# Optimization experiments

Measured on AMD Instinct MI355X. Metric: run time of the kernel, lower is better.

## Reference

```python
import jax, jax.numpy as jnp
import numpy as np

ITERS = 3; S = 8; I = 64; E = 64; C = 64; DIN = 128; SLOT = 128; H = 256
B = 64; N = 4096; EPS = 1e-8

def _ln(x, g, b):
    m = jnp.mean(x, -1, keepdims=True)
    v = jnp.var(x, -1, keepdims=True)
    return (x - m) * jax.lax.rsqrt(v + 1e-5) * g + b

def _gru(x, h, Wih, Whh, bih, bhh):
    # torch nn.GRUCell math; W stored as [in, 3*hidden]
    gi = x @ Wih + bih
    gh = h @ Whh + bhh
    ir, iz, inn = jnp.split(gi, 3, -1)
    hr, hz, hn = jnp.split(gh, 3, -1)
    r = jax.nn.sigmoid(ir + hr)
    z = jax.nn.sigmoid(iz + hz)
    n = jnp.tanh(inn + r * hn)
    return (1.0 - z) * n + z * h

def setup_inputs() -> dict:
    k = jax.random.split(jax.random.key(0), 32)
    d = {}
    d['slots_bck'] = jax.random.normal(k[0], (B, 1, SLOT), jnp.float32)
    d['inputs'] = jax.random.normal(k[1], (B, N, DIN), jnp.float32)
    d['protos'] = jax.random.normal(k[2], (C, I), jnp.float32)
    d['ext_noise'] = jax.random.normal(k[3], (B, S, E), jnp.float32)
    d['int_noise'] = jax.random.normal(k[4], (B, S, C), jnp.float32)
    u = jax.random.uniform(k[5], (ITERS, B, S, C), jnp.float32, 1e-6, 1.0 - 1e-6)
    d['gumbel'] = -jnp.log(-jnp.log(u))
    d['tau'] = 1
    w = lambda i, shape, s=0.05: jax.random.normal(k[i], shape, jnp.float32) * s
    d['ext_mu'] = w(6, (1, 1, E)); d['ext_log_sigma'] = w(7, (1, 1, E))
    d['int_mu'] = w(8, (1, 1, C)); d['int_log_sigma'] = w(9, (1, 1, C))
    d['ln_in_g'] = jnp.ones((DIN,)); d['ln_in_b'] = jnp.zeros((DIN,))
    d['ln_p_g'] = jnp.ones((I,)); d['ln_p_b'] = jnp.zeros((I,))
    d['ln_mi_g'] = jnp.ones((I,)); d['ln_mi_b'] = jnp.zeros((I,))
    d['ln_me_g'] = jnp.ones((E,)); d['ln_me_b'] = jnp.zeros((E,))
    d['Wq'] = w(10, (SLOT, SLOT)); d['Wk'] = w(11, (DIN, SLOT))
    d['Wv'] = w(12, (DIN, SLOT)); d['Wp'] = w(13, (I, I))
    d['gi_Wih'] = w(14, (I, 3 * I)); d['gi_Whh'] = w(15, (I, 3 * I))
    d['gi_bih'] = jnp.zeros((3 * I,)); d['gi_bhh'] = jnp.zeros((3 * I,))
    d['ge_Wih'] = w(16, (E, 3 * E)); d['ge_Whh'] = w(17, (E, 3 * E))
    d['ge_bih'] = jnp.zeros((3 * E,)); d['ge_bhh'] = jnp.zeros((3 * E,))
    d['mi_W1'] = w(18, (I, H)); d['mi_b1'] = jnp.zeros((H,))
    d['mi_W2'] = w(19, (H, I)); d['mi_b2'] = jnp.zeros((I,))
    d['me_W1'] = w(20, (E, H)); d['me_b1'] = jnp.zeros((H,))
    d['me_W2'] = w(21, (H, E)); d['me_b2'] = jnp.zeros((E,))
    return d

def reference(slots_bck, inputs, protos, ext_noise, int_noise, gumbel,
              ext_mu, ext_log_sigma, int_mu, int_log_sigma,
              ln_in_g, ln_in_b, ln_p_g, ln_p_b, ln_mi_g, ln_mi_b, ln_me_g, ln_me_b,
              Wq, Wk, Wv, Wp,
              gi_Wih, gi_Whh, gi_bih, gi_bhh, ge_Wih, ge_Whh, ge_bih, ge_bhh,
              mi_W1, mi_b1, mi_W2, mi_b2, me_W1, me_b1, me_W2, me_b2, tau):
    Bsz = inputs.shape[0]
    slots_ext = ext_mu + jnp.exp(ext_log_sigma) * ext_noise            # [B,S,E]
    logits_pi = int_mu + jnp.exp(int_log_sigma) * int_noise            # [B,S,C]
    x = _ln(inputs, ln_in_g, ln_in_b)
    kk = (x @ Wk) * (SLOT ** -0.5)                                     # [B,N,SLOT]
    vv = x @ Wv                                                        # [B,N,SLOT]
    p = _ln(protos, ln_p_g, ln_p_b) @ Wp                               # [C,I]
    attn_vis = None
    for i in range(ITERS):
        pi = jax.nn.softmax((logits_pi + gumbel[i]) / tau, axis=-1)    # soft gumbel-softmax
        slots_int = pi @ p                                             # [B,S,I]
        slots_obj = jnp.concatenate([slots_int, slots_ext], -1)        # [B,S,SLOT]
        slots = jnp.concatenate([slots_bck, slots_obj[:, 1:]], 1)
        q = slots @ Wq                                                 # [B,S,SLOT]
        attn_logits = jnp.einsum('bnd,bsd->bns', kk, q)
        attn_vis = jax.nn.softmax(attn_logits, -1)                     # softmax over slots
        attn = attn_vis + EPS
        attn = attn / jnp.sum(attn, -2, keepdims=True)                 # renorm over inputs
        updates = jnp.einsum('bns,bnd->bsd', attn, vv)                 # [B,S,SLOT]
        upd_int, upd_ext = updates[..., :I], updates[..., I:]
        slots_ext = _gru(upd_ext.reshape(-1, E), slots_ext.reshape(-1, E),
                         ge_Wih, ge_Whh, ge_bih, ge_bhh).reshape(Bsz, S, E)
        if i < ITERS - 1:
            h = _ln(slots_ext, ln_me_g, ln_me_b)
            slots_ext = slots_ext + (jax.nn.relu(h @ me_W1 + me_b1) @ me_W2 + me_b2)
        int_upd = _gru(upd_int.reshape(-1, I), slots_int.reshape(-1, I),
                       gi_Wih, gi_Whh, gi_bih, gi_bhh).reshape(Bsz, S, I)
        if i < ITERS - 1:
            h = _ln(int_upd, ln_mi_g, ln_mi_b)
            int_upd = int_upd + (jax.nn.relu(h @ mi_W1 + mi_b1) @ mi_W2 + mi_b2)
        logits_pi = (int_upd @ p.T) * (I ** -0.5)
    return slots_ext[:, 1:], logits_pi[:, 1:], attn_vis
```

## Files before the change

### kernel.cpp

```cpp
#include <hip/hip_runtime.h>
#include <stdint.h>

typedef unsigned short u16;
#define DEVFN static __device__ __forceinline__

typedef __attribute__((ext_vector_type(8))) short bf16x8;
typedef __attribute__((ext_vector_type(4))) float f32x4;

constexpr int   kB   = 64;
constexpr int   kN   = 4096;
constexpr float kEPS = 1e-8f;
constexpr float kLNE = 1e-5f;
constexpr float kKSC = 0.08838834764831845f;
constexpr float kISC = 0.125f;

DEVFN float bf2f(uint32_t u) { union { uint32_t u; float f; } x; x.u = u << 16; return x.f; }
DEVFN u16 f2bf(float f) {
    union { float f; uint32_t u; } x; x.f = f;
    uint32_t r = (x.u + 0x7fffu + ((x.u >> 16) & 1u)) >> 16;
    return (u16)r;
}
DEVFN void unpack8(uint4 p, float* d) {
    d[0] = bf2f(p.x & 0xffffu); d[1] = bf2f(p.x >> 16);
    d[2] = bf2f(p.y & 0xffffu); d[3] = bf2f(p.y >> 16);
    d[4] = bf2f(p.z & 0xffffu); d[5] = bf2f(p.z >> 16);
    d[6] = bf2f(p.w & 0xffffu); d[7] = bf2f(p.w >> 16);
}
DEVFN float sigf(float x) { return 1.0f / (1.0f + __expf(-x)); }

__global__ void kinit(const float* __restrict__ ext_mu, const float* __restrict__ ext_ls,
                      const float* __restrict__ int_mu, const float* __restrict__ int_ls,
                      const float* __restrict__ ext_noise, const float* __restrict__ int_noise,
                      float* __restrict__ sext, float* __restrict__ lpi)
{
    int t = blockIdx.x * 256 + threadIdx.x;
    int e = t & 63;
    sext[t] = ext_mu[e] + __expf(ext_ls[e]) * ext_noise[t];
    lpi[t]  = int_mu[e] + __expf(int_ls[e]) * int_noise[t];
}

__global__ void kwprep(const float* __restrict__ Wk, const float* __restrict__ Wv,
                       u16* __restrict__ WT)
{
    int idx = blockIdx.x * 256 + threadIdx.x;
    int k = idx >> 8, c = idx & 255;
    float v = (c < 128) ? Wk[k * 128 + c] * kKSC : Wv[k * 128 + (c - 128)];
    WT[(size_t)c * 128 + k] = f2bf(v);
}

__global__ void kprep(const float* __restrict__ protos, const float* __restrict__ Wp,
                      const float* __restrict__ lpg, const float* __restrict__ lpb,
                      float* __restrict__ p, float* __restrict__ pT)
{
    __shared__ float pl[64][65];
    __shared__ float mS[64], sS[64];
    int t = threadIdx.x;
    for (int idx = t; idx < 64 * 64; idx += 256) pl[idx >> 6][idx & 63] = protos[idx];
    __syncthreads();
    if (t < 64) {
        float sm = 0.f, sq = 0.f;
        for (int k = 0; k < 64; ++k) { float v = pl[t][k]; sm += v; sq += v * v; }
        float m = sm * (1.0f / 64.0f);
        float var = sq * (1.0f / 64.0f) - m * m;
        mS[t] = m; sS[t] = rsqrtf(var + kLNE);
    }
    __syncthreads();
    for (int idx = t; idx < 64 * 64; idx += 256) {
        int r = idx >> 6, c = idx & 63;
        pl[r][c] = (pl[r][c] - mS[r]) * sS[r] * lpg[c] + lpb[c];
    }
    __syncthreads();
    for (int idx = t; idx < 64 * 64; idx += 256) {
        int r = idx >> 6, c = idx & 63;
        float acc = 0.f;
        for (int k = 0; k < 64; ++k) acc += pl[r][k] * Wp[k * 64 + c];
        p[r * 64 + c] = acc;
        pT[c * 64 + r] = acc;
    }
}

__global__ __launch_bounds__(256) void kmain(const float* __restrict__ inputs,
                                             const u16* __restrict__ WT,
                                             const float* __restrict__ lng, const float* __restrict__ lnb,
                                             u16* __restrict__ kk, u16* __restrict__ vv,
                                             float* __restrict__ vpart)
{
    __shared__ u16 At[64 * 128];
    const int t = threadIdx.x;
    const int blk = blockIdx.x;
    const int b = blk >> 6;
    const int n0 = (blk & 63) * 64;
    const float* inp = inputs + ((size_t)(b * kN + n0)) * 128;

    float4 xv[8];
    #pragma unroll
    for (int j = 0; j < 8; ++j) xv[j] = ((const float4*)inp)[t + j * 256];

    float s[8], qq[8];
    #pragma unroll
    for (int j = 0; j < 8; ++j) {
        s[j]  = xv[j].x + xv[j].y + xv[j].z + xv[j].w;
        qq[j] = xv[j].x * xv[j].x + xv[j].y * xv[j].y + xv[j].z * xv[j].z + xv[j].w * xv[j].w;
    }
    #pragma unroll
    for (int d = 16; d >= 1; d >>= 1) {
        #pragma unroll
        for (int j = 0; j < 8; ++j) {
            s[j]  += __shfl_xor(s[j], d);
            qq[j] += __shfl_xor(qq[j], d);
        }
    }
    const int col4 = t & 31;
    const float4 g4 = ((const float4*)lng)[col4];
    const float4 b4 = ((const float4*)lnb)[col4];
    #pragma unroll
    for (int j = 0; j < 8; ++j) {
        const int row = (t >> 5) + 8 * j;
        const float m  = s[j] * (1.0f / 128.0f);
        const float var = qq[j] * (1.0f / 128.0f) - m * m;
        const float sc = rsqrtf(var + kLNE);
        const float a0 = (xv[j].x - m) * sc * g4.x + b4.x;
        const float a1 = (xv[j].y - m) * sc * g4.y + b4.y;
        const float a2 = (xv[j].z - m) * sc * g4.z + b4.z;
        const float a3 = (xv[j].w - m) * sc * g4.w + b4.w;
        uint32_t p0 = (uint32_t)f2bf(a0) | ((uint32_t)f2bf(a1) << 16);
        uint32_t p1 = (uint32_t)f2bf(a2) | ((uint32_t)f2bf(a3) << 16);
        const int byteoff = row * 256 + (((col4 >> 1) ^ (row & 7)) << 4) + ((col4 & 1) << 3);
        *(uint2*)((char*)At + byteoff) = make_uint2(p0, p1);
    }
    __syncthreads();

    const int w   = t >> 6;
    const int l   = t & 63;
    const int lg  = l >> 4;
    const int lr  = l & 15;
    const int wc0 = w * 64;

    f32x4 acc[4][4];
    #pragma unroll
    for (int m = 0; m < 4; ++m)
        #pragma unroll
        for (int n = 0; n < 4; ++n) acc[m][n] = (f32x4){0.f, 0.f, 0.f, 0.f};

    #pragma unroll
    for (int ks = 0; ks < 4; ++ks) {
        bf16x8 afr[4];
        #pragma unroll
        for (int m = 0; m < 4; ++m) {
            const int row = 16 * m + lr;
            const int chunk = (ks * 4 + lg) ^ (row & 7);
            afr[m] = *(const bf16x8*)((const char*)At + row * 256 + chunk * 16);
        }
        #pragma unroll
        for (int n = 0; n < 4; ++n) {
            const int col = wc0 + 16 * n + lr;
            bf16x8 bfr = *(const bf16x8*)(WT + (size_t)col * 128 + ks * 32 + lg * 8);
            #pragma unroll
            for (int m = 0; m < 4; ++m)
                acc[m][n] = __builtin_amdgcn_mfma_f32_16x16x32_bf16(afr[m], bfr, acc[m][n], 0, 0, 0);
        }
    }

    #pragma unroll
    for (int n = 0; n < 4; ++n) {
        const int colg = wc0 + 16 * n + lr;
        u16* basep = (colg < 128) ? kk : vv;
        const int colo = colg & 127;
        #pragma unroll
        for (int m = 0; m < 4; ++m) {
            #pragma unroll
            for (int r = 0; r < 4; ++r) {
                const int row = n0 + 16 * m + lg * 4 + r;
                basep[((size_t)(b * kN) + row) * 128 + colo] = f2bf(acc[m][n][r]);
            }
        }
    }
    if (w >= 2) {
        #pragma unroll
        for (int n = 0; n < 4; ++n) {
            float sv = 0.f;
            #pragma unroll
            for (int m = 0; m < 4; ++m)
                #pragma unroll
                for (int r = 0; r < 4; ++r) sv += acc[m][n][r];
            sv += __shfl_xor(sv, 16);
            sv += __shfl_xor(sv, 32);
            if (lg == 0) vpart[(size_t)blk * 128 + (wc0 - 128) + 16 * n + lr] = sv;
        }
    }
}

__global__ void kvvsum(const float* __restrict__ part, float* __restrict__ vvsum)
{
    int t = blockIdx.x * 256 + threadIdx.x;
    int b = t >> 7, c = t & 127;
    float s = 0.f;
    const float* pp = part + (size_t)b * 64 * 128 + c;
    for (int nb = 0; nb < 64; ++nb) s += pp[nb * 128];
    vvsum[t] = s;
}

__global__ void kslots(const float* __restrict__ lpi, const float* __restrict__ gum,
                       const void* __restrict__ taup,
                       const float* __restrict__ p,
                       const float* __restrict__ sbck, const float* __restrict__ sext,
                       const float* __restrict__ Wq,
                       float* __restrict__ sint, float* __restrict__ q)
{
    __shared__ float piL[64];
    __shared__ float sv[128];
    const int bs = blockIdx.x;
    const int b = bs >> 3, s = bs & 7;
    const int t = threadIdx.x;
    float inv_tau = 1.0f;
    {
        int iv = *(const int*)taup;
        if (iv > 0 && iv < 1000000) inv_tau = 1.0f / (float)iv;
        else {
            float fv = *(const float*)taup;
            if (fv > 1e-6f && fv < 1e6f) inv_tau = 1.0f / fv;
        }
    }
    if (t < 64) {
        float l = (lpi[bs * 64 + t] + gum[bs * 64 + t]) * inv_tau;
        float m = l;
        #pragma unroll
        for (int d = 32; d >= 1; d >>= 1) m = fmaxf(m, __shfl_xor(m, d));
        float e = __expf(l - m);
        float sm = e;
        #pragma unroll
        for (int d = 32; d >= 1; d >>= 1) sm += __shfl_xor(sm, d);
        piL[t] = e / sm;
    }
    __syncthreads();
    if (t < 64) {
        float acc = 0.f;
        for (int c = 0; c < 64; ++c) acc += piL[c] * p[c * 64 + t];
        sint[bs * 64 + t] = acc;
        if (s == 0) {
            sv[t]      = sbck[b * 128 + t];
            sv[64 + t] = sbck[b * 128 + 64 + t];
        } else {
            sv[t]      = acc;
            sv[64 + t] = sext[bs * 64 + t];
        }
    }
    __syncthreads();
    {
        float acc = 0.f;
        for (int k = 0; k < 128; ++k) acc += sv[k] * Wq[k * 128 + t];
        q[bs * 128 + t] = acc;
    }
}

__global__ __launch_bounds__(256) void kattn(const u16* __restrict__ kk, const u16* __restrict__ vv,
                                             const float* __restrict__ q,
                                             float* __restrict__ attn_out,
                                             float* __restrict__ pu, float* __restrict__ pcs,
                                             const int wvis)
{
    __shared__ float qL[8][132];
    __shared__ float kkL[32][132];
    __shared__ float vvL[32][132];
    __shared__ float aL[32 * 8];
    const int t = threadIdx.x;
    const int blk = blockIdx.x;
    const int b = blk >> 4;
    const int nb = blk & 15;
    {
        int idx = t * 4;
        float4 v = *((const float4*)(q + (size_t)b * 1024 + idx));
        *((float4*)&qL[idx >> 7][idx & 127]) = v;
    }
    const int r8 = t >> 3, sl = t & 7;
    const int s2 = t >> 5, dg = t & 31;
    float acc0 = 0.f, acc1 = 0.f, acc2 = 0.f, acc3 = 0.f, cs = 0.f;
    __syncthreads();
    for (int ch = 0; ch < 8; ++ch) {
        const int nbase = nb * 256 + ch * 32;
        const u16* kp = kk + ((size_t)(b * kN + nbase)) * 128;
        const u16* vp = vv + ((size_t)(b * kN + nbase)) * 128;
        #pragma unroll
        for (int rnd = 0; rnd < 2; ++rnd) {
            const int flat = (t + rnd * 256) * 8;
            const int rr = flat >> 7, c0 = flat & 127;
            uint4 pk = *((const uint4*)(kp + flat));
            uint4 pv = *((const uint4*)(vp + flat));
            float fk[8], fvv[8];
            unpack8(pk, fk); unpack8(pv, fvv);
            *((float4*)&kkL[rr][c0])     = make_float4(fk[0], fk[1], fk[2], fk[3]);
            *((float4*)&kkL[rr][c0 + 4]) = make_float4(fk[4], fk[5], fk[6], fk[7]);
            *((float4*)&vvL[rr][c0])     = make_float4(fvv[0], fvv[1], fvv[2], fvv[3]);
            *((float4*)&vvL[rr][c0 + 4]) = make_float4(fvv[4], fvv[5], fvv[6], fvv[7]);
        }
        __syncthreads();
        float lg = 0.f;
        {
            const float4* kr = (const float4*)&kkL[r8][0];
            const float4* qr = (const float4*)&qL[sl][0];
            #pragma unroll 8
            for (int k4 = 0; k4 < 32; ++k4) {
                float4 kx = kr[k4], qx = qr[k4];
                lg = fmaf(kx.x, qx.x, lg); lg = fmaf(kx.y, qx.y, lg);
                lg = fmaf(kx.z, qx.z, lg); lg = fmaf(kx.w, qx.w, lg);
            }
        }
        float m = lg;
        m = fmaxf(m, __shfl_xor(m, 1)); m = fmaxf(m, __shfl_xor(m, 2)); m = fmaxf(m, __shfl_xor(m, 4));
        float e = __expf(lg - m);
        float sm = e;
        sm += __shfl_xor(sm, 1); sm += __shfl_xor(sm, 2); sm += __shfl_xor(sm, 4);
        float av = e / sm;
        if (wvis) attn_out[((size_t)(b * kN + nbase + r8)) * 8 + sl] = av;
        aL[r8 * 8 + sl] = av;
        __syncthreads();
        #pragma unroll 4
        for (int rr = 0; rr < 32; ++rr) {
            float aw = aL[rr * 8 + s2];
            float4 v = *((const float4*)&vvL[rr][dg * 4]);
            acc0 = fmaf(aw, v.x, acc0); acc1 = fmaf(aw, v.y, acc1);
            acc2 = fmaf(aw, v.z, acc2); acc3 = fmaf(aw, v.w, acc3);
            cs += aw;
        }
        __syncthreads();
    }
    *((float4*)(pu + (size_t)blk * 1024 + s2 * 128 + dg * 4)) = make_float4(acc0, acc1, acc2, acc3);
    if (dg == 0) pcs[blk * 8 + s2] = cs;
}

__global__ __launch_bounds__(256) void kupdate(
    const float* __restrict__ pu, const float* __restrict__ pcs,
    const float* __restrict__ vvsum, const float* __restrict__ sint,
    float* __restrict__ sext, float* __restrict__ lpi,
    const float* __restrict__ giWih, const float* __restrict__ giWhh,
    const float* __restrict__ gibih, const float* __restrict__ gibhh,
    const float* __restrict__ geWih, const float* __restrict__ geWhh,
    const float* __restrict__ gebih, const float* __restrict__ gebhh,
    const float* __restrict__ miW1, const float* __restrict__ mib1,
    const float* __restrict__ miW2, const float* __restrict__ mib2,
    const float* __restrict__ meW1, const float* __restrict__ meb1,
    const float* __restrict__ meW2, const float* __restrict__ meb2,
    const float* __restrict__ lmig, const float* __restrict__ lmib,
    const float* __restrict__ lmeg, const float* __restrict__ lmeb,
    const float* __restrict__ pT, float* __restrict__ out, const int last)
{
    __shared__ float uL[128], hA[64], hB[64];
    __shared__ float g1[192], g2[192];
    __shared__ float tmp[256];
    __shared__ float outE[64], outI[64];
    const int bs = blockIdx.x;
    const int b = bs >> 3, s = bs & 7;
    const int t = threadIdx.x;

    if (t < 128) {
        float num = 0.f;
        for (int nb = 0; nb < 16; ++nb) num += pu[((size_t)((b * 16 + nb) * 8 + s)) * 128 + t];
        float den = 4096.0f * kEPS;
        for (int nb = 0; nb < 16; ++nb) den += pcs[(b * 16 + nb) * 8 + s];
        uL[t] = (num + kEPS * vvsum[b * 128 + t]) / den;
    } else if (t < 192) {
        hA[t - 128] = sext[bs * 64 + (t - 128)];
    } else {
        hB[t - 192] = sint[bs * 64 + (t - 192)];
    }
    __syncthreads();
    if (t < 192) {
        float a = gebih[t], bb = gebhh[t];
        for (int k = 0; k < 64; ++k) {
            a  = fmaf(uL[64 + k], geWih[k * 192 + t], a);
            bb = fmaf(hA[k],      geWhh[k * 192 + t], bb);
        }
        g1[t] = a; g2[t] = bb;
    }
    __syncthreads();
    if (t < 64) {
        float r = sigf(g1[t] + g2[t]);
        float z = sigf(g1[64 + t] + g2[64 + t]);
        float nn = tanhf(g1[128 + t] + r * g2[128 + t]);
        outE[t] = (1.0f - z) * nn + z * hA[t];
    }
    __syncthreads();
    if (t < 192) {
        float a = gibih[t], bb = gibhh[t];
        for (int k = 0; k < 64; ++k) {
            a  = fmaf(uL[k], giWih[k * 192 + t], a);
            bb = fmaf(hB[k], giWhh[k * 192 + t], bb);
        }
        g1[t] = a; g2[t] = bb;
    }
    __syncthreads();
    if (t < 64) {
        float r = sigf(g1[t] + g2[t]);
        float z = sigf(g1[64 + t] + g2[64 + t]);
        float nn = tanhf(g1[128 + t] + r * g2[128 + t]);
        outI[t] = (1.0f - z) * nn + z * hB[t];
    }
    __syncthreads();
    if (!last) {
        if (t < 64) {
            float v = outE[t];
            float sm = v, sq = v * v;
            #pragma unroll
            for (int d = 32; d >= 1; d >>= 1) { sm += __shfl_xor(sm, d); sq += __shfl_xor(sq, d); }
            float m = sm * (1.0f / 64.0f), var = sq * (1.0f / 64.0f) - m * m;
            g1[t] = (v - m) * rsqrtf(var + kLNE) * lmeg[t] + lmeb[t];
        }
        __syncthreads();
        {
            float a = meb1[t];
            for (int k = 0; k < 64; ++k) a = fmaf(g1[k], meW1[k * 256 + t], a);
            tmp[t] = fmaxf(a, 0.0f);
        }
        __syncthreads();
        if (t < 64) {
            float o = meb2[t];
            for (int j = 0; j < 256; ++j) o = fmaf(tmp[j], meW2[j * 64 + t], o);
            outE[t] += o;
        }
        __syncthreads();
        if (t < 64) {
            float v = outI[t];
            float sm = v, sq = v * v;
            #pragma unroll
            for (int d = 32; d >= 1; d >>= 1) { sm += __shfl_xor(sm, d); sq += __shfl_xor(sq, d); }
            float m = sm * (1.0f / 64.0f), var = sq * (1.0f / 64.0f) - m * m;
            g1[t] = (v - m) * rsqrtf(var + kLNE) * lmig[t] + lmib[t];
        }
        __syncthreads();
        {
            float a = mib1[t];
            for (int k = 0; k < 64; ++k) a = fmaf(g1[k], miW1[k * 256 + t], a);
            tmp[t] = fmaxf(a, 0.0f);
        }
        __syncthreads();
        if (t < 64) {
            float o = mib2[t];
            for (int j = 0; j < 256; ++j) o = fmaf(tmp[j], miW2[j * 64 + t], o);
            outI[t] += o;
        }
        __syncthreads();
    }
    if (t < 64) {
        float lg = 0.f;
        for (int k = 0; k < 64; ++k) lg = fmaf(outI[k], pT[k * 64 + t], lg);
        lg *= kISC;
        lpi[bs * 64 + t] = lg;
        if (last && s > 0) out[28672 + (b * 7 + (s - 1)) * 64 + t] = lg;
    } else if (t < 128) {
        int c = t - 64;
        float v = outE[c];
        sext[bs * 64 + c] = v;
        if (last && s > 0) out[(b * 7 + (s - 1)) * 64 + c] = v;
    }
}

extern "C" void kernel_launch(void* const* d_in, const int* in_sizes, int n_in,
                              void* d_out, int out_size, void* d_ws, size_t ws_size,
                              hipStream_t stream)
{
    (void)in_sizes; (void)n_in; (void)out_size; (void)ws_size;
    const float* slots_bck = (const float*)d_in[0];
    const float* inputs    = (const float*)d_in[1];
    const float* protos    = (const float*)d_in[2];
    const float* ext_noise = (const float*)d_in[3];
    const float* int_noise = (const float*)d_in[4];
    const float* gumbel    = (const float*)d_in[5];
    const void*  taup      = d_in[6];
    const float* ext_mu    = (const float*)d_in[7];
    const float* ext_ls    = (const float*)d_in[8];
    const float* int_mu    = (const float*)d_in[9];
    const float* int_ls    = (const float*)d_in[10];
    const float* ln_in_g   = (const float*)d_in[11];
    const float* ln_in_b   = (const float*)d_in[12];
    const float* ln_p_g    = (const float*)d_in[13];
    const float* ln_p_b    = (const float*)d_in[14];
    const float* ln_mi_g   = (const float*)d_in[15];
    const float* ln_mi_b   = (const float*)d_in[16];
    const float* ln_me_g   = (const float*)d_in[17];
    const float* ln_me_b   = (const float*)d_in[18];
    const float* Wq        = (const float*)d_in[19];
    const float* Wk        = (const float*)d_in[20];
    const float* Wv        = (const float*)d_in[21];
    const float* Wp        = (const float*)d_in[22];
    const float* giWih     = (const float*)d_in[23];
    const float* giWhh     = (const float*)d_in[24];
    const float* gibih     = (const float*)d_in[25];
    const float* gibhh     = (const float*)d_in[26];
    const float* geWih     = (const float*)d_in[27];
    const float* geWhh     = (const float*)d_in[28];
    const float* gebih     = (const float*)d_in[29];
    const float* gebhh     = (const float*)d_in[30];
    const float* miW1      = (const float*)d_in[31];
    const float* mib1      = (const float*)d_in[32];
    const float* miW2      = (const float*)d_in[33];
    const float* mib2      = (const float*)d_in[34];
    const float* meW1      = (const float*)d_in[35];
    const float* meb1      = (const float*)d_in[36];
    const float* meW2      = (const float*)d_in[37];
    const float* meb2      = (const float*)d_in[38];
    float* out = (float*)d_out;

    char* ws = (char*)d_ws;
    size_t o = 0;
    auto alloc = [&](size_t bytes) { size_t r = o; o += (bytes + 255) & ~(size_t)255; return r; };
    u16*   kkp   = (u16*)  (ws + alloc((size_t)kB * kN * 128 * 2));
    u16*   vvp   = (u16*)  (ws + alloc((size_t)kB * kN * 128 * 2));
    u16*   WT    = (u16*)  (ws + alloc(256 * 128 * 2));
    float* vpart = (float*)(ws + alloc((size_t)4096 * 128 * 4));
    float* vvsum = (float*)(ws + alloc(8192 * 4));
    float* pbuf  = (float*)(ws + alloc(4096 * 4));
    float* pT    = (float*)(ws + alloc(4096 * 4));
    float* sext  = (float*)(ws + alloc(32768 * 4));
    float* lpi   = (float*)(ws + alloc(32768 * 4));
    float* sint  = (float*)(ws + alloc(32768 * 4));
    float* q     = (float*)(ws + alloc(65536 * 4));
    float* pu    = (float*)(ws + alloc((size_t)1024 * 1024 * 4));
    float* pcs   = (float*)(ws + alloc(8192 * 4));

    kinit<<<128, 256, 0, stream>>>(ext_mu, ext_ls, int_mu, int_ls, ext_noise, int_noise, sext, lpi);
    kwprep<<<128, 256, 0, stream>>>(Wk, Wv, WT);
    kprep<<<1, 256, 0, stream>>>(protos, Wp, ln_p_g, ln_p_b, pbuf, pT);
    kmain<<<4096, 256, 0, stream>>>(inputs, WT, ln_in_g, ln_in_b, kkp, vvp, vpart);
    kvvsum<<<32, 256, 0, stream>>>(vpart, vvsum);

    for (int i = 0; i < 3; ++i) {
        kslots<<<512, 128, 0, stream>>>(lpi, gumbel + (size_t)i * 32768, taup, pbuf,
                                        slots_bck, sext, Wq, sint, q);
        kattn<<<1024, 256, 0, stream>>>(kkp, vvp, q, out + 57344, pu, pcs, (i == 2) ? 1 : 0);
        kupdate<<<512, 256, 0, stream>>>(pu, pcs, vvsum, sint, sext, lpi,
                                         giWih, giWhh, gibih, gibhh,
                                         geWih, geWhh, gebih, gebhh,
                                         miW1, mib1, miW2, mib2,
                                         meW1, meb1, meW2, meb2,
                                         ln_mi_g, ln_mi_b, ln_me_g, ln_me_b,
                                         pT, out, (i == 2) ? 1 : 0);
    }
}
```

Baseline: 316.6 us.

## Use MFMA for slot attention and store V transposed for the PV product

The attention kernel moves from scalar fp32 dot products over LDS-staged K/V tiles to bf16 MFMA. One MFMA computes Q·K logits with the softmax done in registers, and a second MFMA accumulates the attention-weighted V sum from a transposed V layout written by the projection kernel. The projection kernel now does the LayerNorm with one row per four threads and stores packed bf16 pairs. Grid size and the partial buffers are halved to match. The intent is to remove the fp32 unpack and FMA cost in the attention loop that runs three times. In exchange the queries and attention weights are rounded to bf16 before the products, and the transposed V stores are strided.

```diff
diff --git a/kernel.cpp b/kernel.cpp
--- a/kernel.cpp
+++ b/kernel.cpp
@@ -1,4 +1,5 @@
 #include <hip/hip_runtime.h>
+#include <hip/hip_bf16.h>
 #include <stdint.h>
 
 typedef unsigned short u16;
@@ -14,17 +15,18 @@
 constexpr float kKSC = 0.08838834764831845f;
 constexpr float kISC = 0.125f;
 
-DEVFN float bf2f(uint32_t u) { union { uint32_t u; float f; } x; x.u = u << 16; return x.f; }
 DEVFN u16 f2bf(float f) {
     union { float f; uint32_t u; } x; x.f = f;
     uint32_t r = (x.u + 0x7fffu + ((x.u >> 16) & 1u)) >> 16;
     return (u16)r;
 }
-DEVFN void unpack8(uint4 p, float* d) {
-    d[0] = bf2f(p.x & 0xffffu); d[1] = bf2f(p.x >> 16);
-    d[2] = bf2f(p.y & 0xffffu); d[3] = bf2f(p.y >> 16);
-    d[4] = bf2f(p.z & 0xffffu); d[5] = bf2f(p.z >> 16);
-    d[6] = bf2f(p.w & 0xffffu); d[7] = bf2f(p.w >> 16);
+DEVFN uint32_t pk2(float lo, float hi) {
+    __hip_bfloat162 h = __float22bfloat162_rn(make_float2(lo, hi));
+    uint32_t u; __builtin_memcpy(&u, &h, 4); return u;
+}
+DEVFN u16 bf1(float f) {
+    __hip_bfloat16 h = __float2bfloat16(f);
+    u16 u; __builtin_memcpy(&u, &h, 2); return u;
 }
 DEVFN float sigf(float x) { return 1.0f / (1.0f + __expf(-x)); }
 
@@ -82,7 +84,7 @@
 __global__ __launch_bounds__(256) void kmain(const float* __restrict__ inputs,
                                              const u16* __restrict__ WT,
                                              const float* __restrict__ lng, const float* __restrict__ lnb,
-                                             u16* __restrict__ kk, u16* __restrict__ vv,
+                                             u16* __restrict__ kk, u16* __restrict__ vvT,
                                              float* __restrict__ vpart)
 {
     __shared__ u16 At[64 * 128];
@@ -92,100 +94,111 @@
     const int n0 = (blk & 63) * 64;
     const float* inp = inputs + ((size_t)(b * kN + n0)) * 128;
 
+    const int row = t >> 2, q4 = t & 3;
     float4 xv[8];
     #pragma unroll
-    for (int j = 0; j < 8; ++j) xv[j] = ((const float4*)inp)[t + j * 256];
-
-    float s[8], qq[8];
+    for (int j = 0; j < 8; ++j) xv[j] = ((const float4*)inp)[row * 32 + q4 * 8 + j];
+
+    float sm = 0.f, sq = 0.f;
     #pragma unroll
     for (int j = 0; j < 8; ++j) {
-        s[j]  = xv[j].x + xv[j].y + xv[j].z + xv[j].w;
-        qq[j] = xv[j].x * xv[j].x + xv[j].y * xv[j].y + xv[j].z * xv[j].z + xv[j].w * xv[j].w;
-    }
-    #pragma unroll
-    for (int d = 16; d >= 1; d >>= 1) {
-        #pragma unroll
-        for (int j = 0; j < 8; ++j) {
-            s[j]  += __shfl_xor(s[j], d);
-            qq[j] += __shfl_xor(qq[j], d);
-        }
-    }
-    const int col4 = t & 31;
-    const float4 g4 = ((const float4*)lng)[col4];
-    const float4 b4 = ((const float4*)lnb)[col4];
-    #pragma unroll
-    for (int j = 0; j < 8; ++j) {
-        const int row = (t >> 5) + 8 * j;
-        const float m  = s[j] * (1.0f / 128.0f);
-        const float var = qq[j] * (1.0f / 128.0f) - m * m;
-        const float sc = rsqrtf(var + kLNE);
-        const float a0 = (xv[j].x - m) * sc * g4.x + b4.x;
-        const float a1 = (xv[j].y - m) * sc * g4.y + b4.y;
-        const float a2 = (xv[j].z - m) * sc * g4.z + b4.z;
-        const float a3 = (xv[j].w - m) * sc * g4.w + b4.w;
-        uint32_t p0 = (uint32_t)f2bf(a0) | ((uint32_t)f2bf(a1) << 16);
-        uint32_t p1 = (uint32_t)f2bf(a2) | ((uint32_t)f2bf(a3) << 16);
-        const int byteoff = row * 256 + (((col4 >> 1) ^ (row & 7)) << 4) + ((col4 & 1) << 3);
-        *(uint2*)((char*)At + byteoff) = make_uint2(p0, p1);
-    }
-    __syncthreads();
-
-    const int w   = t >> 6;
-    const int l   = t & 63;
-    const int lg  = l >> 4;
-    const int lr  = l & 15;
-    const int wc0 = w * 64;
+        sm += xv[j].x + xv[j].y + xv[j].z + xv[j].w;
+        sq += xv[j].x * xv[j].x + xv[j].y * xv[j].y + xv[j].z * xv[j].z + xv[j].w * xv[j].w;
+    }
+    sm += __shfl_xor(sm, 1); sm += __shfl_xor(sm, 2);
+    sq += __shfl_xor(sq, 1); sq += __shfl_xor(sq, 2);
+    const float mn  = sm * (1.0f / 128.0f);
+    const float var = sq * (1.0f / 128.0f) - mn * mn;
+    const float sc  = rsqrtf(var + kLNE);
+
+    const float4* g4p = ((const float4*)lng) + q4 * 8;
+    const float4* b4p = ((const float4*)lnb) + q4 * 8;
+    #pragma unroll
+    for (int jj = 0; jj < 4; ++jj) {
+        const float4 a0 = xv[jj * 2], a1 = xv[jj * 2 + 1];
+        const float4 g0 = g4p[jj * 2], g1 = g4p[jj * 2 + 1];
+        const float4 c0 = b4p[jj * 2], c1 = b4p[jj * 2 + 1];
+        uint4 pk;
+        pk.x = pk2((a0.x - mn) * sc * g0.x + c0.x, (a0.y - mn) * sc * g0.y + c0.y);
+        pk.y = pk2((a0.z - mn) * sc * g0.z + c0.z, (a0.w - mn) * sc * g0.w + c0.w);
+        pk.z = pk2((a1.x - mn) * sc * g1.x + c1.x, (a1.y - mn) * sc * g1.y + c1.y);
+        pk.w = pk2((a1.z - mn) * sc * g1.z + c1.z, (a1.w - mn) * sc * g1.w + c1.w);
+        const int chunk = (q4 * 4 + jj) ^ (row & 7);
+        *(uint4*)((char*)At + row * 256 + chunk * 16) = pk;
+    }
+    __syncthreads();
+
+    const int w  = t >> 6;
+    const int l  = t & 63;
+    const int lg = l >> 4;
+    const int lr = l & 15;
+    const bool iskk = (w < 2);
 
     f32x4 acc[4][4];
     #pragma unroll
-    for (int m = 0; m < 4; ++m)
-        #pragma unroll
-        for (int n = 0; n < 4; ++n) acc[m][n] = (f32x4){0.f, 0.f, 0.f, 0.f};
+    for (int i = 0; i < 4; ++i)
+        #pragma unroll
+        for (int j = 0; j < 4; ++j) acc[i][j] = (f32x4){0.f, 0.f, 0.f, 0.f};
 
     #pragma unroll
     for (int ks = 0; ks < 4; ++ks) {
-        bf16x8 afr[4];
-        #pragma unroll
-        for (int m = 0; m < 4; ++m) {
-            const int row = 16 * m + lr;
-            const int chunk = (ks * 4 + lg) ^ (row & 7);
-            afr[m] = *(const bf16x8*)((const char*)At + row * 256 + chunk * 16);
-        }
-        #pragma unroll
-        for (int n = 0; n < 4; ++n) {
-            const int col = wc0 + 16 * n + lr;
-            bf16x8 bfr = *(const bf16x8*)(WT + (size_t)col * 128 + ks * 32 + lg * 8);
-            #pragma unroll
-            for (int m = 0; m < 4; ++m)
-                acc[m][n] = __builtin_amdgcn_mfma_f32_16x16x32_bf16(afr[m], bfr, acc[m][n], 0, 0, 0);
-        }
-    }
-
-    #pragma unroll
-    for (int n = 0; n < 4; ++n) {
-        const int colg = wc0 + 16 * n + lr;
-        u16* basep = (colg < 128) ? kk : vv;
-        const int colo = colg & 127;
-        #pragma unroll
-        for (int m = 0; m < 4; ++m) {
-            #pragma unroll
-            for (int r = 0; r < 4; ++r) {
-                const int row = n0 + 16 * m + lg * 4 + r;
-                basep[((size_t)(b * kN) + row) * 128 + colo] = f2bf(acc[m][n][r]);
+        bf16x8 wf[4], xf[4];
+        #pragma unroll
+        for (int i = 0; i < 4; ++i)
+            wf[i] = *(const bf16x8*)(WT + (size_t)(w * 64 + 16 * i + lr) * 128 + ks * 32 + lg * 8);
+        #pragma unroll
+        for (int i = 0; i < 4; ++i) {
+            const int r2 = 16 * i + lr;
+            const int chunk = (ks * 4 + lg) ^ (r2 & 7);
+            xf[i] = *(const bf16x8*)((const char*)At + r2 * 256 + chunk * 16);
+        }
+        if (iskk) {
+            #pragma unroll
+            for (int i = 0; i < 4; ++i)
+                #pragma unroll
+                for (int j = 0; j < 4; ++j)
+                    acc[i][j] = __builtin_amdgcn_mfma_f32_16x16x32_bf16(wf[i], xf[j], acc[i][j], 0, 0, 0);
+        } else {
+            #pragma unroll
+            for (int i = 0; i < 4; ++i)
+                #pragma unroll
+                for (int j = 0; j < 4; ++j)
+                    acc[i][j] = __builtin_amdgcn_mfma_f32_16x16x32_bf16(xf[i], wf[j], acc[i][j], 0, 0, 0);
+        }
+    }
+
+    if (iskk) {
+        #pragma unroll
+        for (int nn = 0; nn < 4; ++nn) {
+            const size_t rb = ((size_t)(b * kN) + n0 + 16 * nn + lr) * 128;
+            #pragma unroll
+            for (int cm = 0; cm < 4; ++cm) {
+                uint2 pk;
+                pk.x = pk2(acc[cm][nn][0], acc[cm][nn][1]);
+                pk.y = pk2(acc[cm][nn][2], acc[cm][nn][3]);
+                *(uint2*)(kk + rb + w * 64 + 16 * cm + lg * 4) = pk;
             }
         }
-    }
-    if (w >= 2) {
-        #pragma unroll
-        for (int n = 0; n < 4; ++n) {
+    } else {
+        #pragma unroll
+        for (int ct = 0; ct < 4; ++ct) {
+            const int d = (w - 2) * 64 + 16 * ct + lr;
+            const size_t db = ((size_t)b * 128 + d) * (size_t)kN;
+            #pragma unroll
+            for (int m = 0; m < 4; ++m) {
+                uint2 pk;
+                pk.x = pk2(acc[m][ct][0], acc[m][ct][1]);
+                pk.y = pk2(acc[m][ct][2], acc[m][ct][3]);
+                *(uint2*)(vvT + db + n0 + 16 * m + lg * 4) = pk;
+            }
             float sv = 0.f;
             #pragma unroll
             for (int m = 0; m < 4; ++m)
                 #pragma unroll
-                for (int r = 0; r < 4; ++r) sv += acc[m][n][r];
+                for (int r = 0; r < 4; ++r) sv += acc[m][ct][r];
             sv += __shfl_xor(sv, 16);
             sv += __shfl_xor(sv, 32);
-            if (lg == 0) vpart[(size_t)blk * 128 + (wc0 - 128) + 16 * n + lr] = sv;
+            if (lg == 0) vpart[(size_t)blk * 128 + d] = sv;
         }
     }
 }
@@ -227,10 +240,10 @@
         #pragma unroll
         for (int d = 32; d >= 1; d >>= 1) m = fmaxf(m, __shfl_xor(m, d));
         float e = __expf(l - m);
-        float sm = e;
-        #pragma unroll
-        for (int d = 32; d >= 1; d >>= 1) sm += __shfl_xor(sm, d);
-        piL[t] = e / sm;
+        float smv = e;
+        #pragma unroll
+        for (int d = 32; d >= 1; d >>= 1) smv += __shfl_xor(smv, d);
+        piL[t] = e / smv;
     }
     __syncthreads();
     if (t < 64) {
@@ -253,79 +266,114 @@
     }
 }
 
-__global__ __launch_bounds__(256) void kattn(const u16* __restrict__ kk, const u16* __restrict__ vv,
+__global__ __launch_bounds__(256) void kattn(const u16* __restrict__ kk, const u16* __restrict__ vvT,
                                              const float* __restrict__ q,
                                              float* __restrict__ attn_out,
                                              float* __restrict__ pu, float* __restrict__ pcs,
                                              const int wvis)
 {
-    __shared__ float qL[8][132];
-    __shared__ float kkL[32][132];
-    __shared__ float vvL[32][132];
-    __shared__ float aL[32 * 8];
+    __shared__ u16 qbf[16][128];
+    __shared__ u16 aB[4][16][40];
+    __shared__ float pwU[4][8][132];
+    __shared__ float csL[4][8];
     const int t = threadIdx.x;
     const int blk = blockIdx.x;
-    const int b = blk >> 4;
-    const int nb = blk & 15;
+    const int b = blk >> 3;
+    const int nb = blk & 7;
+    const int w = t >> 6, l = t & 63, lg = l >> 4, lr = l & 15;
+
     {
-        int idx = t * 4;
-        float4 v = *((const float4*)(q + (size_t)b * 1024 + idx));
-        *((float4*)&qL[idx >> 7][idx & 127]) = v;
-    }
-    const int r8 = t >> 3, sl = t & 7;
-    const int s2 = t >> 5, dg = t & 31;
-    float acc0 = 0.f, acc1 = 0.f, acc2 = 0.f, acc3 = 0.f, cs = 0.f;
-    __syncthreads();
-    for (int ch = 0; ch < 8; ++ch) {
-        const int nbase = nb * 256 + ch * 32;
-        const u16* kp = kk + ((size_t)(b * kN + nbase)) * 128;
-        const u16* vp = vv + ((size_t)(b * kN + nbase)) * 128;
-        #pragma unroll
-        for (int rnd = 0; rnd < 2; ++rnd) {
-            const int flat = (t + rnd * 256) * 8;
-            const int rr = flat >> 7, c0 = flat & 127;
-            uint4 pk = *((const uint4*)(kp + flat));
-            uint4 pv = *((const uint4*)(vp + flat));
-            float fk[8], fvv[8];
-            unpack8(pk, fk); unpack8(pv, fvv);
-            *((float4*)&kkL[rr][c0])     = make_float4(fk[0], fk[1], fk[2], fk[3]);
-            *((float4*)&kkL[rr][c0 + 4]) = make_float4(fk[4], fk[5], fk[6], fk[7]);
-            *((float4*)&vvL[rr][c0])     = make_float4(fvv[0], fvv[1], fvv[2], fvv[3]);
-            *((float4*)&vvL[rr][c0 + 4]) = make_float4(fvv[4], fvv[5], fvv[6], fvv[7]);
-        }
-        __syncthreads();
-        float lg = 0.f;
-        {
-            const float4* kr = (const float4*)&kkL[r8][0];
-            const float4* qr = (const float4*)&qL[sl][0];
-            #pragma unroll 8
-            for (int k4 = 0; k4 < 32; ++k4) {
-                float4 kx = kr[k4], qx = qr[k4];
-                lg = fmaf(kx.x, qx.x, lg); lg = fmaf(kx.y, qx.y, lg);
-                lg = fmaf(kx.z, qx.z, lg); lg = fmaf(kx.w, qx.w, lg);
+        float4 v = ((const float4*)(q + (size_t)b * 1024))[t];
+        uint2 pk;
+        pk.x = pk2(v.x, v.y);
+        pk.y = pk2(v.z, v.w);
+        *(uint2*)&qbf[t >> 5][(t & 31) * 4] = pk;
+        ((uint32_t*)qbf)[512 + t] = 0u;
+        ((uint32_t*)qbf)[768 + (t & 255)] = 0u;
+    }
+    __syncthreads();
+
+    bf16x8 qf[4];
+    #pragma unroll
+    for (int ks = 0; ks < 4; ++ks) qf[ks] = *(const bf16x8*)&qbf[lr][ks * 32 + lg * 8];
+
+    f32x4 apv[8];
+    #pragma unroll
+    for (int dt = 0; dt < 8; ++dt) apv[dt] = (f32x4){0.f, 0.f, 0.f, 0.f};
+    float cs0 = 0.f, cs1 = 0.f, cs2 = 0.f, cs3 = 0.f;
+
+    const size_t kkb = (size_t)(b * kN) * 128;
+    const size_t vvb = (size_t)b * 128 * (size_t)kN;
+
+    for (int ch = 0; ch < 4; ++ch) {
+        const int nbase = nb * 512 + w * 128 + ch * 32;
+        #pragma unroll
+        for (int c2 = 0; c2 < 2; ++c2) {
+            const int n16 = nbase + 16 * c2;
+            f32x4 pl = (f32x4){0.f, 0.f, 0.f, 0.f};
+            #pragma unroll
+            for (int ks = 0; ks < 4; ++ks) {
+                bf16x8 bfr = *(const bf16x8*)(kk + kkb + (size_t)(n16 + lr) * 128 + ks * 32 + lg * 8);
+                pl = __builtin_amdgcn_mfma_f32_16x16x32_bf16(qf[ks], bfr, pl, 0, 0, 0);
             }
-        }
-        float m = lg;
-        m = fmaxf(m, __shfl_xor(m, 1)); m = fmaxf(m, __shfl_xor(m, 2)); m = fmaxf(m, __shfl_xor(m, 4));
-        float e = __expf(lg - m);
-        float sm = e;
-        sm += __shfl_xor(sm, 1); sm += __shfl_xor(sm, 2); sm += __shfl_xor(sm, 4);
-        float av = e / sm;
-        if (wvis) attn_out[((size_t)(b * kN + nbase + r8)) * 8 + sl] = av;
-        aL[r8 * 8 + sl] = av;
-        __syncthreads();
-        #pragma unroll 4
-        for (int rr = 0; rr < 32; ++rr) {
-            float aw = aL[rr * 8 + s2];
-            float4 v = *((const float4*)&vvL[rr][dg * 4]);
-            acc0 = fmaf(aw, v.x, acc0); acc1 = fmaf(aw, v.y, acc1);
-            acc2 = fmaf(aw, v.z, acc2); acc3 = fmaf(aw, v.w, acc3);
-            cs += aw;
-        }
-        __syncthreads();
-    }
-    *((float4*)(pu + (size_t)blk * 1024 + s2 * 128 + dg * 4)) = make_float4(acc0, acc1, acc2, acc3);
-    if (dg == 0) pcs[blk * 8 + s2] = cs;
+            float m = fmaxf(fmaxf(pl[0], pl[1]), fmaxf(pl[2], pl[3]));
+            m = fmaxf(m, __shfl_xor(m, 16));
+            float e0 = __expf(pl[0] - m), e1 = __expf(pl[1] - m);
+            float e2 = __expf(pl[2] - m), e3 = __expf(pl[3] - m);
+            float smv = e0 + e1 + e2 + e3;
+            smv += __shfl_xor(smv, 16);
+            const float inv = 1.0f / smv;
+            const float a0 = e0 * inv, a1 = e1 * inv, a2 = e2 * inv, a3 = e3 * inv;
+            if (lg < 2) {
+                cs0 += a0; cs1 += a1; cs2 += a2; cs3 += a3;
+                if (wvis)
+                    *(float4*)(attn_out + ((size_t)(b * kN) + n16 + lr) * 8 + lg * 4) =
+                        make_float4(a0, a1, a2, a3);
+                const int s0 = lg * 4, nn = 16 * c2 + lr;
+                aB[w][s0 + 0][nn] = bf1(a0);
+                aB[w][s0 + 1][nn] = bf1(a1);
+                aB[w][s0 + 2][nn] = bf1(a2);
+                aB[w][s0 + 3][nn] = bf1(a3);
+            }
+        }
+        bf16x8 af = *(const bf16x8*)&aB[w][lr][lg * 8];
+        #pragma unroll
+        for (int dt = 0; dt < 8; ++dt) {
+            bf16x8 vfr = *(const bf16x8*)(vvT + vvb + (size_t)(16 * dt + lr) * kN + nbase + lg * 8);
+            apv[dt] = __builtin_amdgcn_mfma_f32_16x16x32_bf16(vfr, af, apv[dt], 0, 0, 0);
+        }
+    }
+
+    if (lr < 8) {
+        #pragma unroll
+        for (int dt = 0; dt < 8; ++dt)
+            *(float4*)&pwU[w][lr][16 * dt + lg * 4] =
+                make_float4(apv[dt][0], apv[dt][1], apv[dt][2], apv[dt][3]);
+    }
+    #pragma unroll
+    for (int d = 8; d >= 1; d >>= 1) {
+        cs0 += __shfl_xor(cs0, d); cs1 += __shfl_xor(cs1, d);
+        cs2 += __shfl_xor(cs2, d); cs3 += __shfl_xor(cs3, d);
+    }
+    if (lr == 0 && lg < 2) {
+        csL[w][lg * 4 + 0] = cs0; csL[w][lg * 4 + 1] = cs1;
+        csL[w][lg * 4 + 2] = cs2; csL[w][lg * 4 + 3] = cs3;
+    }
+    __syncthreads();
+    {
+        const int s = t >> 5, dq = t & 31;
+        float4 r0 = *(const float4*)&pwU[0][s][dq * 4];
+        float4 r1 = *(const float4*)&pwU[1][s][dq * 4];
+        float4 r2 = *(const float4*)&pwU[2][s][dq * 4];
+        float4 r3 = *(const float4*)&pwU[3][s][dq * 4];
+        float4 o;
+        o.x = r0.x + r1.x + r2.x + r3.x;
+        o.y = r0.y + r1.y + r2.y + r3.y;
+        o.z = r0.z + r1.z + r2.z + r3.z;
+        o.w = r0.w + r1.w + r2.w + r3.w;
+        *(float4*)(pu + (size_t)blk * 1024 + s * 128 + dq * 4) = o;
+    }
+    if (t < 8) pcs[blk * 8 + t] = csL[0][t] + csL[1][t] + csL[2][t] + csL[3][t];
 }
 
 __global__ __launch_bounds__(256) void kupdate(
@@ -354,9 +402,9 @@
 
     if (t < 128) {
         float num = 0.f;
-        for (int nb = 0; nb < 16; ++nb) num += pu[((size_t)((b * 16 + nb) * 8 + s)) * 128 + t];
+        for (int nb = 0; nb < 8; ++nb) num += pu[((size_t)(b * 8 + nb)) * 1024 + s * 128 + t];
         float den = 4096.0f * kEPS;
-        for (int nb = 0; nb < 16; ++nb) den += pcs[(b * 16 + nb) * 8 + s];
+        for (int nb = 0; nb < 8; ++nb) den += pcs[(b * 8 + nb) * 8 + s];
         uL[t] = (num + kEPS * vvsum[b * 128 + t]) / den;
     } else if (t < 192) {
         hA[t - 128] = sext[bs * 64 + (t - 128)];
@@ -504,7 +552,7 @@
     size_t o = 0;
     auto alloc = [&](size_t bytes) { size_t r = o; o += (bytes + 255) & ~(size_t)255; return r; };
     u16*   kkp   = (u16*)  (ws + alloc((size_t)kB * kN * 128 * 2));
-    u16*   vvp   = (u16*)  (ws + alloc((size_t)kB * kN * 128 * 2));
+    u16*   vvTp  = (u16*)  (ws + alloc((size_t)kB * kN * 128 * 2));
     u16*   WT    = (u16*)  (ws + alloc(256 * 128 * 2));
     float* vpart = (float*)(ws + alloc((size_t)4096 * 128 * 4));
     float* vvsum = (float*)(ws + alloc(8192 * 4));
@@ -514,19 +562,19 @@
     float* lpi   = (float*)(ws + alloc(32768 * 4));
     float* sint  = (float*)(ws + alloc(32768 * 4));
     float* q     = (float*)(ws + alloc(65536 * 4));
-    float* pu    = (float*)(ws + alloc((size_t)1024 * 1024 * 4));
-    float* pcs   = (float*)(ws + alloc(8192 * 4));
+    float* pu    = (float*)(ws + alloc((size_t)512 * 1024 * 4));
+    float* pcs   = (float*)(ws + alloc(512 * 8 * 4));
 
     kinit<<<128, 256, 0, stream>>>(ext_mu, ext_ls, int_mu, int_ls, ext_noise, int_noise, sext, lpi);
     kwprep<<<128, 256, 0, stream>>>(Wk, Wv, WT);
     kprep<<<1, 256, 0, stream>>>(protos, Wp, ln_p_g, ln_p_b, pbuf, pT);
-    kmain<<<4096, 256, 0, stream>>>(inputs, WT, ln_in_g, ln_in_b, kkp, vvp, vpart);
+    kmain<<<4096, 256, 0, stream>>>(inputs, WT, ln_in_g, ln_in_b, kkp, vvTp, vpart);
     kvvsum<<<32, 256, 0, stream>>>(vpart, vvsum);
 
     for (int i = 0; i < 3; ++i) {
         kslots<<<512, 128, 0, stream>>>(lpi, gumbel + (size_t)i * 32768, taup, pbuf,
                                         slots_bck, sext, Wq, sint, q);
-        kattn<<<1024, 256, 0, stream>>>(kkp, vvp, q, out + 57344, pu, pcs, (i == 2) ? 1 : 0);
+        kattn<<<512, 256, 0, stream>>>(kkp, vvTp, q, out + 57344, pu, pcs, (i == 2) ? 1 : 0);
         kupdate<<<512, 256, 0, stream>>>(pu, pcs, vvsum, sint, sext, lpi,
                                          giWih, giWhh, gibih, gibhh,
                                          geWih, geWhh, gebih, gebhh,
```

After: 318.0 us. About the same (+0.5%).
